# Optimization experiments

Hardware: AMD Instinct MI355X
Metric: run time of the kernel (lower is better)

Reference implementation:

```python
import jax, jax.numpy as jnp
from jax import lax
import numpy as np

STATE_DIM = 64
CHANNELS = 128
SEQ_LEN = 4096
BATCH = 16
DT_MIN, DT_MAX = 1e-3, 1e-1


def hippo(n):
    # HiPPO-LegS construction, matching the torch staticmethod
    ar = jnp.arange(n, dtype=jnp.float32)
    P = jnp.sqrt(1.0 + 2.0 * ar)
    A = P[:, None] * P[None, :]
    A = jnp.tril(A) - jnp.diag(ar)
    B = jnp.sqrt(2.0 * ar + 1.0)
    return -A, B[:, None]


def setup_inputs() -> dict:
    key = jax.random.key(0)
    k_u, k_c = jax.random.split(key)
    A, B = hippo(STATE_DIM)
    # xavier_normal_ for C: std = sqrt(2/(fan_in+fan_out))
    std = float(np.sqrt(2.0 / (CHANNELS + STATE_DIM)))
    C = jax.random.normal(k_c, (CHANNELS, STATE_DIM), dtype=jnp.float32) * std
    D = jnp.ones((CHANNELS, 1), dtype=jnp.float32)
    # deterministic dt at log-midpoint of [dt_min, dt_max]
    dt = jnp.exp(jnp.array([(np.log(DT_MIN) + np.log(DT_MAX)) / 2.0], dtype=jnp.float32))
    u = jax.random.normal(k_u, (BATCH, SEQ_LEN), dtype=jnp.float32)
    return {"u": u, "A": A, "B": B, "C": C, "D": D, "dt": dt}


def reference(u, A, B, C, D, dt):
    # Training-path forward of LinearStateSpaceLayer (conv-kernel construction + conv1d)
    b, L = u.shape
    n = A.shape[0]
    dt_s = dt[0]
    I = jnp.eye(n, dtype=A.dtype)
    BL = jnp.linalg.inv(I - 0.5 * dt_s * A)            # bilinear discretization
    A_bar = BL @ (I + 0.5 * dt_s * A)                  # (n, n)
    B_bar = (BL * dt_s) @ B                            # (n, 1)

    # kernel k[j] = C @ A_bar^j @ B_bar for j = 0..L-1, via a scan of matvecs
    def step(v, _):
        return A_bar @ v, v
    _, vs = lax.scan(step, B_bar[:, 0], None, length=L)  # (L, n), vs[j] = A_bar^j B_bar
    k_causal = vs @ C.T                                  # (L, channels)
    # torch ordering: k_conv[c, 0, i] = C A_bar^{L-1-i} B_bar = k_causal[L-1-i, c]
    k_conv = k_causal[::-1].T[:, None, :]                # (channels, 1, L)

    # torch F.conv1d is cross-correlation; lax conv_general_dilated matches
    y = lax.conv_general_dilated(
        u[:, None, :], k_conv,
        window_strides=(1,), padding=[(L - 1, L - 1)],
        dimension_numbers=("NCH", "OIH", "NCH"),
    )[:, :, :L]                                          # (b, channels, L)

    # skip term: (u.unsqueeze(-1) @ D.T).transpose(-1,-2) == u[b,t] * D[c,0]
    y = y + u[:, None, :] * D[None, :, :]                # (b, channels, L)
    return y
```

## Files before the change

### kernel.cpp

```cpp
#include <hip/hip_runtime.h>

#define NS   64
#define CH   128
#define LSEQ 4096
#define NB   16
#define SCH  64
#define MCH  64
#define ST   68
#define CP   128

#define WS_ABAR 0
#define WS_A16  4096
#define WS_VS   8192
#define WS_BBAR 12288

#define X0_IDX(b, m) (((size_t)(b) * CH) * LSEQ + (size_t)(m) * SCH)

#define P_VSS  0
#define P_XCW  1024
#define P_XBS  1280
#define P_PLE  1536
#define P_PART 1792
#define P_A16  2048

#define FMA44(av, bv)                                                          \
    a0.x += av.x * bv.x; a0.y += av.x * bv.y; a0.z += av.x * bv.z; a0.w += av.x * bv.w; \
    a1.x += av.y * bv.x; a1.y += av.y * bv.y; a1.z += av.y * bv.z; a1.w += av.y * bv.w; \
    a2.x += av.z * bv.x; a2.y += av.z * bv.y; a2.z += av.z * bv.z; a2.w += av.z * bv.w; \
    a3.x += av.w * bv.x; a3.y += av.w * bv.y; a3.z += av.w * bv.z; a3.w += av.w * bv.w;

template<bool WT>
__device__ __forceinline__ void mm_square(const float* __restrict__ cm,
                                          const float* __restrict__ cmt,
                                          float* __restrict__ nm,
                                          float* __restrict__ nmt, int e) {
    const int l = e & 63;
    const int si0 = 16 * ((e >> 6) & 3) + 4 * (l >> 4);
    const int sj0 = 4 * (l & 15);
    float4 a0 = {0,0,0,0}, a1 = {0,0,0,0}, a2 = {0,0,0,0}, a3 = {0,0,0,0};
#pragma unroll 4
    for (int k = 0; k < NS; k += 4) {
        float4 av0 = *(const float4*)&cmt[(k + 0) * ST + si0];
        float4 bv0 = *(const float4*)&cm [(k + 0) * ST + sj0];
        float4 av1 = *(const float4*)&cmt[(k + 1) * ST + si0];
        float4 bv1 = *(const float4*)&cm [(k + 1) * ST + sj0];
        float4 av2 = *(const float4*)&cmt[(k + 2) * ST + si0];
        float4 bv2 = *(const float4*)&cm [(k + 2) * ST + sj0];
        float4 av3 = *(const float4*)&cmt[(k + 3) * ST + si0];
        float4 bv3 = *(const float4*)&cm [(k + 3) * ST + sj0];
        FMA44(av0, bv0)
        FMA44(av1, bv1)
        FMA44(av2, bv2)
        FMA44(av3, bv3)
    }
    *(float4*)&nm[(si0 + 0) * ST + sj0] = a0;
    *(float4*)&nm[(si0 + 1) * ST + sj0] = a1;
    *(float4*)&nm[(si0 + 2) * ST + sj0] = a2;
    *(float4*)&nm[(si0 + 3) * ST + sj0] = a3;
    if (WT) {
        float4 t0 = {a0.x, a1.x, a2.x, a3.x};
        float4 t1 = {a0.y, a1.y, a2.y, a3.y};
        float4 t2 = {a0.z, a1.z, a2.z, a3.z};
        float4 t3 = {a0.w, a1.w, a2.w, a3.w};
        *(float4*)&nmt[(sj0 + 0) * ST + si0] = t0;
        *(float4*)&nmt[(sj0 + 1) * ST + si0] = t1;
        *(float4*)&nmt[(sj0 + 2) * ST + si0] = t2;
        *(float4*)&nmt[(sj0 + 3) * ST + si0] = t3;
    }
}

__device__ __forceinline__ void mm_sq42(const float* __restrict__ cm,
                                        const float* __restrict__ cmt,
                                        float* __restrict__ nm,
                                        float* __restrict__ nmt, int tid) {
    const int si0 = 4 * (tid >> 5);
    const int sj0 = 2 * (tid & 31);
    float2 a0 = {0,0}, a1 = {0,0}, a2 = {0,0}, a3 = {0,0};
#pragma unroll 8
    for (int k = 0; k < NS; ++k) {
        float4 av = *(const float4*)&cmt[k * ST + si0];
        float2 bv = *(const float2*)&cm [k * ST + sj0];
        a0.x += av.x * bv.x; a0.y += av.x * bv.y;
        a1.x += av.y * bv.x; a1.y += av.y * bv.y;
        a2.x += av.z * bv.x; a2.y += av.z * bv.y;
        a3.x += av.w * bv.x; a3.y += av.w * bv.y;
    }
    *(float2*)&nm[(si0 + 0) * ST + sj0] = a0;
    *(float2*)&nm[(si0 + 1) * ST + sj0] = a1;
    *(float2*)&nm[(si0 + 2) * ST + sj0] = a2;
    *(float2*)&nm[(si0 + 3) * ST + sj0] = a3;
    float4 t0 = {a0.x, a1.x, a2.x, a3.x};
    float4 t1 = {a0.y, a1.y, a2.y, a3.y};
    *(float4*)&nmt[(sj0 + 0) * ST + si0] = t0;
    *(float4*)&nmt[(sj0 + 1) * ST + si0] = t1;
}

__device__ __forceinline__ void vs_expand1(const float* __restrict__ cmt,
                                           float* __restrict__ VT,
                                           int iq, int j, int mexp) {
    const int i0 = 4 * iq;
    float4 acc = {0,0,0,0};
#pragma unroll 8
    for (int k = 0; k < NS; ++k) {
        float4 av = *(const float4*)&cmt[k * ST + i0];
        float bk = VT[k * ST + j];
        acc.x += av.x * bk; acc.y += av.y * bk;
        acc.z += av.z * bk; acc.w += av.w * bk;
    }
    VT[(i0 + 0) * ST + mexp + j] = acc.x;
    VT[(i0 + 1) * ST + mexp + j] = acc.y;
    VT[(i0 + 2) * ST + mexp + j] = acc.z;
    VT[(i0 + 3) * ST + mexp + j] = acc.w;
}

__device__ __forceinline__ void pq_step(const float* __restrict__ Acol,
                                        const float* __restrict__ xle,
                                        float* __restrict__ outb, int r0, int e) {
    const int g = e >> 4, i0 = 4 * (e & 15);
    const float* bp = &xle[(4 * g + r0) * NS];
    float4 acc = *(const float4*)&xle[(4 * g + r0 + 1) * NS + i0];
#pragma unroll 8
    for (int k = 0; k < NS; ++k) {
        float4 av = *(const float4*)&Acol[k * ST + i0];
        float bk = bp[k];
        acc.x = fmaf(av.x, bk, acc.x); acc.y = fmaf(av.y, bk, acc.y);
        acc.z = fmaf(av.z, bk, acc.z); acc.w = fmaf(av.w, bk, acc.w);
    }
    *(float4*)&outb[g * ST + i0] = acc;
}

__device__ __forceinline__ void y_step(const float* __restrict__ A128col,
                                       const float* __restrict__ P,
                                       const float* __restrict__ Q,
                                       float* __restrict__ Y, int e) {
    const int g = e >> 4, i0 = 4 * (e & 15);
    const float* bp = &P[g * ST];
    float4 acc = *(const float4*)&Q[g * ST + i0];
#pragma unroll 8
    for (int k = 0; k < NS; ++k) {
        float4 av = *(const float4*)&A128col[k * ST + i0];
        float bk = bp[k];
        acc.x = fmaf(av.x, bk, acc.x); acc.y = fmaf(av.y, bk, acc.y);
        acc.z = fmaf(av.z, bk, acc.z); acc.w = fmaf(av.w, bk, acc.w);
    }
    *(float4*)&Y[g * ST + i0] = acc;
}

__device__ __forceinline__ void inner_step(const float* __restrict__ Acol,
                                           const float* __restrict__ xle,
                                           float* __restrict__ stash, int r, int e) {
    const int g = e >> 4, i0 = 4 * (e & 15);
    const int mp = 4 * g + r - 1;
    float4 acc = *(const float4*)&xle[mp * NS + i0];
    const float* xp = &stash[mp * ST];
#pragma unroll 8
    for (int k = 0; k < NS; ++k) {
        float4 av = *(const float4*)&Acol[k * ST + i0];
        float xk = xp[k];
        acc.x = fmaf(av.x, xk, acc.x); acc.y = fmaf(av.y, xk, acc.y);
        acc.z = fmaf(av.z, xk, acc.z); acc.w = fmaf(av.w, xk, acc.w);
    }
    *(float4*)&stash[(mp + 1) * ST + i0] = acc;
}

__device__ __forceinline__ void e1u_step(const float* __restrict__ A128col,
                                         const float* __restrict__ P,
                                         float* __restrict__ stash, int e) {
    const int g = e >> 4, i0 = 4 * (e & 15);
    const float* xp = &stash[(4 * g) * ST];
    float4 acc = *(const float4*)&P[g * ST + i0];
#pragma unroll 8
    for (int k = 0; k < NS; ++k) {
        float4 av = *(const float4*)&A128col[k * ST + i0];
        float xk = xp[k];
        acc.x = fmaf(av.x, xk, acc.x); acc.y = fmaf(av.y, xk, acc.y);
        acc.z = fmaf(av.z, xk, acc.z); acc.w = fmaf(av.w, xk, acc.w);
    }
    *(float4*)&stash[(4 * g + 2) * ST + i0] = acc;
}

__global__ __launch_bounds__(512) void k_sb(const float* __restrict__ u,
                                            const float* __restrict__ A,
                                            const float* __restrict__ Bv,
                                            const float* __restrict__ dtp,
                                            float* __restrict__ ws,
                                            float* __restrict__ out) {
    __shared__ __align__(16) float Mrow[NS * ST];
    __shared__ __align__(16) float Mcol[(NS + 1) * ST];
    __shared__ __align__(16) float Nrow[NS * ST];
    __shared__ __align__(16) float Ncol[NS * ST];
    __shared__ __align__(16) float VT[NS * ST];
    __shared__ __align__(16) float uT[NS * ST];
    __shared__ __align__(16) float vsS[NS * NS];
    __shared__ __align__(16) float xleS[MCH * NS];
    __shared__ __align__(16) float part[2][4 * NS];
    __shared__ __align__(16) float bcol[NS];
    __shared__ float rdiag[NS], xcS[NS];
    float* const stash = uT;
    float* const HbP = vsS;
    float* const HbQ = vsS + 16 * ST;
    float* const HbY = vsS + 32 * ST;
    const int tid = threadIdx.x;
    const int b = blockIdx.x;
    const float dt = dtp[0];
    const float hdt = 0.5f * dt;

    for (int o = tid; o < NS * NS; o += 512) {
        int i = o >> 6, k = o & 63;
        float a = A[o];
        float d = (i == k) ? 1.0f : 0.0f;
        Nrow[i * ST + k] = d - hdt * a;
        Ncol[k * ST + i] = d + hdt * a;
    }
    if (tid < NS) {
        bcol[tid]  = dt * Bv[tid];
        rdiag[tid] = 1.0f / (1.0f - hdt * A[tid * NS + tid]);
    }
    __syncthreads();

    {
        const int jj = tid & 63;
#pragma unroll
        for (int rep = 0; rep < 2; ++rep) {
            const int m0 = 4 * (tid >> 6) + 32 * rep;
            float4 v;
            v.x = u[b * LSEQ + (m0 + 0) * SCH + 63 - jj];
            v.y = u[b * LSEQ + (m0 + 1) * SCH + 63 - jj];
            v.z = u[b * LSEQ + (m0 + 2) * SCH + 63 - jj];
            v.w = u[b * LSEQ + (m0 + 3) * SCH + 63 - jj];
            *(float4*)&uT[jj * ST + m0] = v;
        }
    }

    if (tid <= NS) {
        float xr[NS];
        const float* t2b = (tid < NS) ? &Ncol[tid * ST] : bcol;
#pragma unroll
        for (int I = 0; I < 16; ++I) {
            const int i0 = 4 * I;
            float4 t2 = *(const float4*)&t2b[i0];
            float a0 = t2.x, a1 = t2.y, a2 = t2.z, a3 = t2.w;
#pragma unroll
            for (int k = 0; k < i0; k += 4) {
                float4 n0 = *(const float4*)&Nrow[(i0 + 0) * ST + k];
                float4 n1 = *(const float4*)&Nrow[(i0 + 1) * ST + k];
                float4 n2 = *(const float4*)&Nrow[(i0 + 2) * ST + k];
                float4 n3 = *(const float4*)&Nrow[(i0 + 3) * ST + k];
                a0 -= n0.x * xr[k] + n0.y * xr[k + 1] + n0.z * xr[k + 2] + n0.w * xr[k + 3];
                a1 -= n1.x * xr[k] + n1.y * xr[k + 1] + n1.z * xr[k + 2] + n1.w * xr[k + 3];
                a2 -= n2.x * xr[k] + n2.y * xr[k + 1] + n2.z * xr[k + 2] + n2.w * xr[k + 3];
                a3 -= n3.x * xr[k] + n3.y * xr[k + 1] + n3.z * xr[k + 2] + n3.w * xr[k + 3];
            }
            float4 rd  = *(const float4*)&rdiag[i0];
            float4 nb1 = *(const float4*)&Nrow[(i0 + 1) * ST + i0];
            float4 nb2 = *(const float4*)&Nrow[(i0 + 2) * ST + i0];
            float4 nb3 = *(const float4*)&Nrow[(i0 + 3) * ST + i0];
            float x0 = a0 * rd.x;
            float x1 = (a1 - nb1.x * x0) * rd.y;
            float x2 = (a2 - nb2.x * x0 - nb2.y * x1) * rd.z;
            float x3 = (a3 - nb3.x * x0 - nb3.y * x1 - nb3.z * x2) * rd.w;
            xr[i0 + 0] = x0; xr[i0 + 1] = x1; xr[i0 + 2] = x2; xr[i0 + 3] = x3;
        }
        float* xrow = &Mcol[tid * ST];
#pragma unroll
        for (int k = 0; k < NS; k += 4) {
            float4 v = {xr[k], xr[k + 1], xr[k + 2], xr[k + 3]};
            *(float4*)&xrow[k] = v;
        }
    }
    __syncthreads();

    if (tid < 256) {
        const int i0 = 4 * (tid >> 4), j0 = 4 * (tid & 15);
        float4 r0 = *(const float4*)&Mcol[(j0 + 0) * ST + i0];
        float4 r1 = *(const float4*)&Mcol[(j0 + 1) * ST + i0];
        float4 r2 = *(const float4*)&Mcol[(j0 + 2) * ST + i0];
        float4 r3 = *(const float4*)&Mcol[(j0 + 3) * ST + i0];
        float4 w0 = {r0.x, r1.x, r2.x, r3.x};
        float4 w1 = {r0.y, r1.y, r2.y, r3.y};
        float4 w2 = {r0.z, r1.z, r2.z, r3.z};
        float4 w3 = {r0.w, r1.w, r2.w, r3.w};
        *(float4*)&Mrow[(i0 + 0) * ST + j0] = w0;
        *(float4*)&Mrow[(i0 + 1) * ST + j0] = w1;
        *(float4*)&Mrow[(i0 + 2) * ST + j0] = w2;
        *(float4*)&Mrow[(i0 + 3) * ST + j0] = w3;
        if (b == 0) {
            *(float4*)&ws[WS_ABAR + (i0 + 0) * NS + j0] = w0;
            *(float4*)&ws[WS_ABAR + (i0 + 1) * NS + j0] = w1;
            *(float4*)&ws[WS_ABAR + (i0 + 2) * NS + j0] = w2;
            *(float4*)&ws[WS_ABAR + (i0 + 3) * NS + j0] = w3;
        }
    }
    if (b == 0 && tid < 16)
        *(float4*)&ws[WS_BBAR + 4 * tid] = *(const float4*)&Mcol[NS * ST + 4 * tid];
    if (tid < NS) VT[tid * ST + 0] = Mcol[NS * ST + tid];
    __syncthreads();

    float *cm = Mrow, *cmt = Mcol, *nm = Nrow, *nmt = Ncol;
    for (int s = 1; s <= 6; ++s) {
        if (s <= 4) {
            mm_sq42(cm, cmt, nm, nmt, tid);
            const int mexp = 1 << (s - 1);
            if (tid < 16 * mexp) {
                vs_expand1(cmt, VT, tid & 15, tid >> 4, mexp);
            }
        } else if (tid < 256) {
            mm_square<true>(cm, cmt, nm, nmt, tid);
        } else {
            const int e = tid - 256;
            const int iq = e & 15;
            if (s == 5) {
                vs_expand1(cmt, VT, iq, e >> 4, 16);
            } else {
                const int j0 = 2 * (e >> 4);
                const int i0 = 4 * iq;
                float4 c0 = {0,0,0,0}, c1 = {0,0,0,0};
#pragma unroll 8
                for (int k = 0; k < NS; ++k) {
                    float4 av = *(const float4*)&cmt[k * ST + i0];
                    float2 bv = *(const float2*)&VT[k * ST + j0];
                    c0.x += av.x * bv.x; c0.y += av.y * bv.x;
                    c0.z += av.z * bv.x; c0.w += av.w * bv.x;
                    c1.x += av.x * bv.y; c1.y += av.y * bv.y;
                    c1.z += av.z * bv.y; c1.w += av.w * bv.y;
                }
                float2 w0 = {c0.x, c1.x}, w1 = {c0.y, c1.y};
                float2 w2 = {c0.z, c1.z}, w3 = {c0.w, c1.w};
                *(float2*)&VT[(i0 + 0) * ST + 32 + j0] = w0;
                *(float2*)&VT[(i0 + 1) * ST + 32 + j0] = w1;
                *(float2*)&VT[(i0 + 2) * ST + 32 + j0] = w2;
                *(float2*)&VT[(i0 + 3) * ST + 32 + j0] = w3;
            }
        }
        __syncthreads();
        { float* t = cm; cm = nm; nm = t; t = cmt; cmt = nmt; nmt = t; }
        if (s == 4 && b == 0) {
            for (int o = tid; o < (NS * NS) / 4; o += 512) {
                int r = o >> 4, c4 = (o & 15) * 4;
                *(float4*)&ws[WS_A16 + r * NS + c4] = *(const float4*)&cm[r * ST + c4];
            }
        }
    }

    if (tid < 256) {
        const int i0 = 4 * (tid >> 4), j0 = 4 * (tid & 15);
        float4 v0 = *(const float4*)&VT[(i0 + 0) * ST + j0];
        float4 v1 = *(const float4*)&VT[(i0 + 1) * ST + j0];
        float4 v2 = *(const float4*)&VT[(i0 + 2) * ST + j0];
        float4 v3 = *(const float4*)&VT[(i0 + 3) * ST + j0];
        float4 w0 = {v0.x, v1.x, v2.x, v3.x};
        float4 w1 = {v0.y, v1.y, v2.y, v3.y};
        float4 w2 = {v0.z, v1.z, v2.z, v3.z};
        float4 w3 = {v0.w, v1.w, v2.w, v3.w};
        *(float4*)&vsS[(j0 + 0) * NS + i0] = w0;
        *(float4*)&vsS[(j0 + 1) * NS + i0] = w1;
        *(float4*)&vsS[(j0 + 2) * NS + i0] = w2;
        *(float4*)&vsS[(j0 + 3) * NS + i0] = w3;
        if (b == 0) {
            *(float4*)&ws[WS_VS + (j0 + 0) * NS + i0] = w0;
            *(float4*)&ws[WS_VS + (j0 + 1) * NS + i0] = w1;
            *(float4*)&ws[WS_VS + (j0 + 2) * NS + i0] = w2;
            *(float4*)&ws[WS_VS + (j0 + 3) * NS + i0] = w3;
        }
    } else {
        mm_square<true>(Mrow, Mcol, Nrow, Ncol, tid - 256);
    }
    __syncthreads();

    if (tid < 256) {
        const int ig = tid & 15, mg = tid >> 4;
        float4 a0 = {0,0,0,0}, a1 = {0,0,0,0}, a2 = {0,0,0,0}, a3 = {0,0,0,0};
#pragma unroll 4
        for (int j = 0; j < NS; j += 2) {
            float4 am  = *(const float4*)&uT[j * ST + 4 * mg];
            float4 bi  = *(const float4*)&vsS[j * NS + 4 * ig];
            float4 am2 = *(const float4*)&uT[(j + 1) * ST + 4 * mg];
            float4 bi2 = *(const float4*)&vsS[(j + 1) * NS + 4 * ig];
            FMA44(am, bi)
            FMA44(am2, bi2)
        }
        *(float4*)&xleS[(4 * mg + 0) * NS + 4 * ig] = a0;
        *(float4*)&xleS[(4 * mg + 1) * NS + 4 * ig] = a1;
        *(float4*)&xleS[(4 * mg + 2) * NS + 4 * ig] = a2;
        *(float4*)&xleS[(4 * mg + 3) * NS + 4 * ig] = a3;
    } else {
        mm_square<false>(Nrow, Ncol, VT, VT, tid - 256);
    }
    __syncthreads();

    float4 a256[4];
    if (tid < 256) {
        const int i = tid & 63, q = tid >> 6;
#pragma unroll
        for (int kq = 0; kq < 4; ++kq)
            a256[kq] = *(const float4*)&VT[i * ST + 16 * q + 4 * kq];
        pq_step(Mcol, xleS, HbP, 0, tid);
    } else {
        pq_step(Mcol, xleS, HbQ, 2, tid - 256);
    }
    __syncthreads();

    if (tid < 256) {
        y_step(Ncol, HbP, HbQ, HbY, tid);
    } else if (tid < 320) {
        xcS[tid - 256] = 0.f;
        stash[tid - 256] = 0.f;
    }
    __syncthreads();

    {
        const int i = tid & 63, q = (tid >> 6) & 3;
        for (int g = 0; g < 15; ++g) {
            if (tid < 256) {
                float4 t0 = *(const float4*)(xcS + 16 * q + 0);
                float4 t1 = *(const float4*)(xcS + 16 * q + 4);
                float4 t2 = *(const float4*)(xcS + 16 * q + 8);
                float4 t3 = *(const float4*)(xcS + 16 * q + 12);
                float s = a256[0].x * t0.x + a256[0].y * t0.y + a256[0].z * t0.z + a256[0].w * t0.w
                        + a256[1].x * t1.x + a256[1].y * t1.y + a256[1].z * t1.z + a256[1].w * t1.w
                        + a256[2].x * t2.x + a256[2].y * t2.y + a256[2].z * t2.z + a256[2].w * t2.w
                        + a256[3].x * t3.x + a256[3].y * t3.y + a256[3].z * t3.z + a256[3].w * t3.w;
                part[g & 1][q * 64 + i] = s;
            }
            __syncthreads();
            if (tid < 256) {
                float xn = part[g & 1][i] + part[g & 1][64 + i] + part[g & 1][128 + i]
                         + part[g & 1][192 + i] + HbY[g * ST + i];
                xcS[i] = xn;
                stash[(4 * g + 4) * ST + i] = xn;
            }
        }
    }
    __syncthreads();

    if (tid < 256) inner_step(Mcol, xleS, stash, 1, tid);
    else           e1u_step(Ncol, HbP, stash, tid - 256);
    __syncthreads();

    if (tid < 256) inner_step(Mcol, xleS, stash, 3, tid);
    __syncthreads();

    {
        const int m = tid >> 3, t8 = (tid & 7) * 8;
        float4 o1 = *(const float4*)&stash[m * ST + t8];
        float4 o2 = *(const float4*)&stash[m * ST + t8 + 4];
        *(float4*)&out[X0_IDX(b, m) + t8]     = o1;
        *(float4*)&out[X0_IDX(b, m) + t8 + 4] = o2;
    }
}

__global__ __launch_bounds__(256) void k_main2(const float* __restrict__ u,
                                               const float* __restrict__ Cm,
                                               const float* __restrict__ Dv,
                                               const float* __restrict__ ws,
                                               float* __restrict__ out) {
    __shared__ __align__(16) float Xl[NS * ST];
    __shared__ __align__(16) float pool[NS * CP];
    __shared__ float uS[SCH], DS[CH], bbS[NS];
    const int m = blockIdx.x, b = blockIdx.y;
    const int tid = threadIdx.x;
    const int l = tid & 63, w = tid >> 6;

    for (int o = tid; o < (NS * NS) / 4; o += 256) {
        int r = o >> 4, c4 = (o & 15) * 4;
        *(float4*)&Xl[r * ST + c4]          = *(const float4*)&ws[WS_ABAR + r * NS + c4];
        *(float4*)&pool[P_A16 + r * NS + c4] = *(const float4*)&ws[WS_A16 + r * NS + c4];
    }
    for (int o = tid; o < 16 * NS; o += 256) pool[P_VSS + o] = ws[WS_VS + o];
    if (tid < NS) {
        uS[tid]  = u[b * LSEQ + m * SCH + tid];
        bbS[tid] = ws[WS_BBAR + tid];
        pool[P_XBS + tid] = out[X0_IDX(b, m) + tid];
    }
    if (tid < CH) DS[tid] = Dv[tid];
    __syncthreads();

    const int r0 = l & 15, q = l >> 4;
    float4 ar[4][4];
#pragma unroll
    for (int b4 = 0; b4 < 4; ++b4)
#pragma unroll
        for (int kq = 0; kq < 4; ++kq)
            ar[b4][kq] = *(const float4*)&Xl[(r0 + 16 * b4) * ST + 16 * q + 4 * kq];
    float bbr[4];
#pragma unroll
    for (int b4 = 0; b4 < 4; ++b4) bbr[b4] = bbS[r0 + 16 * b4];
    float4 a16r[4];
#pragma unroll
    for (int kq = 0; kq < 4; ++kq)
        a16r[kq] = *(const float4*)&pool[P_A16 + l * NS + 16 * w + 4 * kq];

    {
        float s = 0.f;
#pragma unroll
        for (int j = 0; j < 16; ++j) s += pool[P_VSS + j * NS + l] * uS[16 * w + 15 - j];
        pool[P_PLE + w * NS + l] = s;
    }
    __syncthreads();

    for (int p = 1; p < 4; ++p) {
        float4 x0q = *(const float4*)&pool[P_XBS + (p - 1) * NS + 16 * w + 0];
        float4 x1q = *(const float4*)&pool[P_XBS + (p - 1) * NS + 16 * w + 4];
        float4 x2q = *(const float4*)&pool[P_XBS + (p - 1) * NS + 16 * w + 8];
        float4 x3q = *(const float4*)&pool[P_XBS + (p - 1) * NS + 16 * w + 12];
        float s = a16r[0].x * x0q.x + a16r[0].y * x0q.y + a16r[0].z * x0q.z + a16r[0].w * x0q.w
                + a16r[1].x * x1q.x + a16r[1].y * x1q.y + a16r[1].z * x1q.z + a16r[1].w * x1q.w
                + a16r[2].x * x2q.x + a16r[2].y * x2q.y + a16r[2].z * x2q.z + a16r[2].w * x2q.w
                + a16r[3].x * x3q.x + a16r[3].y * x3q.y + a16r[3].z * x3q.z + a16r[3].w * x3q.w;
        pool[P_PART + w * NS + l] = s;
        __syncthreads();
        if (w == 0) {
            float xn = pool[P_PART + l] + pool[P_PART + NS + l] + pool[P_PART + 2 * NS + l]
                     + pool[P_PART + 3 * NS + l] + pool[P_PLE + (p - 1) * NS + l];
            pool[P_XBS + p * NS + l] = xn;
        }
        __syncthreads();
    }

    pool[P_XCW + w * NS + l] = pool[P_XBS + w * NS + l];
    for (int s = 0; s < 16; ++s) {
        __threadfence_block();
        const int t = 16 * w + s;
        float4 x0q = *(const float4*)&pool[P_XCW + w * NS + 16 * q + 0];
        float4 x1q = *(const float4*)&pool[P_XCW + w * NS + 16 * q + 4];
        float4 x2q = *(const float4*)&pool[P_XCW + w * NS + 16 * q + 8];
        float4 x3q = *(const float4*)&pool[P_XCW + w * NS + 16 * q + 12];
        float p0, p1, p2, p3;
        p0 = ar[0][0].x * x0q.x + ar[0][0].y * x0q.y + ar[0][0].z * x0q.z + ar[0][0].w * x0q.w
           + ar[0][1].x * x1q.x + ar[0][1].y * x1q.y + ar[0][1].z * x1q.z + ar[0][1].w * x1q.w
           + ar[0][2].x * x2q.x + ar[0][2].y * x2q.y + ar[0][2].z * x2q.z + ar[0][2].w * x2q.w
           + ar[0][3].x * x3q.x + ar[0][3].y * x3q.y + ar[0][3].z * x3q.z + ar[0][3].w * x3q.w;
        p1 = ar[1][0].x * x0q.x + ar[1][0].y * x0q.y + ar[1][0].z * x0q.z + ar[1][0].w * x0q.w
           + ar[1][1].x * x1q.x + ar[1][1].y * x1q.y + ar[1][1].z * x1q.z + ar[1][1].w * x1q.w
           + ar[1][2].x * x2q.x + ar[1][2].y * x2q.y + ar[1][2].z * x2q.z + ar[1][2].w * x2q.w
           + ar[1][3].x * x3q.x + ar[1][3].y * x3q.y + ar[1][3].z * x3q.z + ar[1][3].w * x3q.w;
        p2 = ar[2][0].x * x0q.x + ar[2][0].y * x0q.y + ar[2][0].z * x0q.z + ar[2][0].w * x0q.w
           + ar[2][1].x * x1q.x + ar[2][1].y * x1q.y + ar[2][1].z * x1q.z + ar[2][1].w * x1q.w
           + ar[2][2].x * x2q.x + ar[2][2].y * x2q.y + ar[2][2].z * x2q.z + ar[2][2].w * x2q.w
           + ar[2][3].x * x3q.x + ar[2][3].y * x3q.y + ar[2][3].z * x3q.z + ar[2][3].w * x3q.w;
        p3 = ar[3][0].x * x0q.x + ar[3][0].y * x0q.y + ar[3][0].z * x0q.z + ar[3][0].w * x0q.w
           + ar[3][1].x * x1q.x + ar[3][1].y * x1q.y + ar[3][1].z * x1q.z + ar[3][1].w * x1q.w
           + ar[3][2].x * x2q.x + ar[3][2].y * x2q.y + ar[3][2].z * x2q.z + ar[3][2].w * x2q.w
           + ar[3][3].x * x3q.x + ar[3][3].y * x3q.y + ar[3][3].z * x3q.z + ar[3][3].w * x3q.w;
        p0 += __shfl_xor(p0, 16, 64); p1 += __shfl_xor(p1, 16, 64);
        p2 += __shfl_xor(p2, 16, 64); p3 += __shfl_xor(p3, 16, 64);
        p0 += __shfl_xor(p0, 32, 64); p1 += __shfl_xor(p1, 32, 64);
        p2 += __shfl_xor(p2, 32, 64); p3 += __shfl_xor(p3, 32, 64);
        const float ut = uS[t];
        p0 += bbr[0] * ut; p1 += bbr[1] * ut; p2 += bbr[2] * ut; p3 += bbr[3] * ut;
        const float xv = (q == 0) ? p0 : (q == 1) ? p1 : (q == 2) ? p2 : p3;
        const int row = r0 + 16 * q;
        pool[P_XCW + w * NS + row] = xv;
        Xl[row * ST + t] = xv;
    }
    __syncthreads();

#pragma unroll
    for (int rep = 0; rep < 8; ++rep) {
        const int ii = tid & 63;
        const int cg = (tid >> 6) + 4 * rep;
        float4 v;
        v.x = Cm[(4 * cg + 0) * NS + ii];
        v.y = Cm[(4 * cg + 1) * NS + ii];
        v.z = Cm[(4 * cg + 2) * NS + ii];
        v.w = Cm[(4 * cg + 3) * NS + ii];
        *(float4*)&pool[ii * CP + 4 * cg] = v;
    }
    __syncthreads();

    {
        const int tg = tid & 7, cq = tid >> 3;
        float acc[4][8];
#pragma unroll
        for (int r = 0; r < 4; ++r)
#pragma unroll
            for (int c = 0; c < 8; ++c) acc[r][c] = 0.f;
#pragma unroll 4
        for (int ii = 0; ii < NS; ++ii) {
            float4 cv = *(const float4*)&pool[ii * CP + 4 * cq];
            float4 xa = *(const float4*)&Xl[ii * ST + 8 * tg + 0];
            float4 xb = *(const float4*)&Xl[ii * ST + 8 * tg + 4];
            float cr[4] = {cv.x, cv.y, cv.z, cv.w};
            float xv[8] = {xa.x, xa.y, xa.z, xa.w, xb.x, xb.y, xb.z, xb.w};
#pragma unroll
            for (int r = 0; r < 4; ++r)
#pragma unroll
                for (int c = 0; c < 8; ++c) acc[r][c] += cr[r] * xv[c];
        }
        const size_t obase = ((size_t)b * CH) * LSEQ + (size_t)m * SCH + 8 * tg;
#pragma unroll
        for (int r = 0; r < 4; ++r) {
            const int c = 4 * cq + r;
            const float dv = DS[c];
            float4 o1, o2;
            o1.x = acc[r][0] + dv * uS[8 * tg + 0];
            o1.y = acc[r][1] + dv * uS[8 * tg + 1];
            o1.z = acc[r][2] + dv * uS[8 * tg + 2];
            o1.w = acc[r][3] + dv * uS[8 * tg + 3];
            o2.x = acc[r][4] + dv * uS[8 * tg + 4];
            o2.y = acc[r][5] + dv * uS[8 * tg + 5];
            o2.z = acc[r][6] + dv * uS[8 * tg + 6];
            o2.w = acc[r][7] + dv * uS[8 * tg + 7];
            float* op = out + obase + (size_t)c * LSEQ;
            *(float4*)(op)     = o1;
            *(float4*)(op + 4) = o2;
        }
    }
}

extern "C" void kernel_launch(void* const* d_in, const int* in_sizes, int n_in,
                              void* d_out, int out_size, void* d_ws, size_t ws_size,
                              hipStream_t stream) {
    const float* u   = (const float*)d_in[0];
    const float* A   = (const float*)d_in[1];
    const float* Bv  = (const float*)d_in[2];
    const float* Cm  = (const float*)d_in[3];
    const float* Dv  = (const float*)d_in[4];
    const float* dtp = (const float*)d_in[5];
    float* ws  = (float*)d_ws;
    float* out = (float*)d_out;

    k_sb<<<NB, 512, 0, stream>>>(u, A, Bv, dtp, ws, out);
    k_main2<<<dim3(MCH, NB), 256, 0, stream>>>(u, Cm, Dv, ws, out);
}
```

Baseline: 154.3 us.

## Shorten serial chunk-state recurrence to 7 steps using A^512 and 3-level expansion

The serial block-level recurrence over chunk states now strides by 8 chunks using a precomputed A^512 power (one extra matrix squaring, which also stores the transposed A^256) instead of 15 steps with A^256. The intermediate chunk states are then filled in by a three-stage tree expansion with new row/column matvec helpers. The matrix-square loops are cut to a triangular k range, assuming lower-triangular powers. Workspace writes are also spread across blocks 1-3 instead of all coming from block 0. This trades fewer serialized, barrier-bound steps for more shared memory (an extra 64x68 buffer) and extra parallel matvec work.

Result: no change. 154.4 us (+0.1%).

```diff
diff --git a/kernel.cpp b/kernel.cpp
--- a/kernel.cpp
+++ b/kernel.cpp
@@ -29,6 +29,7 @@
     a2.x += av.z * bv.x; a2.y += av.z * bv.y; a2.z += av.z * bv.z; a2.w += av.z * bv.w; \
     a3.x += av.w * bv.x; a3.y += av.w * bv.y; a3.z += av.w * bv.z; a3.w += av.w * bv.w;
 
+
 template<bool WT>
 __device__ __forceinline__ void mm_square(const float* __restrict__ cm,
                                           const float* __restrict__ cmt,
@@ -37,9 +38,9 @@
     const int l = e & 63;
     const int si0 = 16 * ((e >> 6) & 3) + 4 * (l >> 4);
     const int sj0 = 4 * (l & 15);
+    const int kmax = si0 + 4;
     float4 a0 = {0,0,0,0}, a1 = {0,0,0,0}, a2 = {0,0,0,0}, a3 = {0,0,0,0};
-#pragma unroll 4
-    for (int k = 0; k < NS; k += 4) {
+    for (int k = 0; k < kmax; k += 4) {
         float4 av0 = *(const float4*)&cmt[(k + 0) * ST + si0];
         float4 bv0 = *(const float4*)&cm [(k + 0) * ST + sj0];
         float4 av1 = *(const float4*)&cmt[(k + 1) * ST + si0];
@@ -75,9 +76,10 @@
                                         float* __restrict__ nmt, int tid) {
     const int si0 = 4 * (tid >> 5);
     const int sj0 = 2 * (tid & 31);
+    const int kmax = si0 + 4;
     float2 a0 = {0,0}, a1 = {0,0}, a2 = {0,0}, a3 = {0,0};
-#pragma unroll 8
-    for (int k = 0; k < NS; ++k) {
+#pragma unroll 4
+    for (int k = 0; k < kmax; ++k) {
         float4 av = *(const float4*)&cmt[k * ST + si0];
         float2 bv = *(const float2*)&cm [k * ST + sj0];
         a0.x += av.x * bv.x; a0.y += av.x * bv.y;
@@ -146,37 +148,33 @@
     *(float4*)&Y[g * ST + i0] = acc;
 }
 
-__device__ __forceinline__ void inner_step(const float* __restrict__ Acol,
-                                           const float* __restrict__ xle,
-                                           float* __restrict__ stash, int r, int e) {
-    const int g = e >> 4, i0 = 4 * (e & 15);
-    const int mp = 4 * g + r - 1;
-    float4 acc = *(const float4*)&xle[mp * NS + i0];
-    const float* xp = &stash[mp * ST];
+__device__ __forceinline__ void exp8u(const float* __restrict__ Pcol,
+                                      const float* __restrict__ addRow,
+                                      const float* __restrict__ srcRow,
+                                      float* __restrict__ dstRow, int i0) {
+    float4 acc = *(const float4*)&addRow[i0];
 #pragma unroll 8
     for (int k = 0; k < NS; ++k) {
-        float4 av = *(const float4*)&Acol[k * ST + i0];
-        float xk = xp[k];
+        float4 av = *(const float4*)&Pcol[k * ST + i0];
+        float xk = srcRow[k];
         acc.x = fmaf(av.x, xk, acc.x); acc.y = fmaf(av.y, xk, acc.y);
         acc.z = fmaf(av.z, xk, acc.z); acc.w = fmaf(av.w, xk, acc.w);
     }
-    *(float4*)&stash[(mp + 1) * ST + i0] = acc;
-}
-
-__device__ __forceinline__ void e1u_step(const float* __restrict__ A128col,
-                                         const float* __restrict__ P,
-                                         float* __restrict__ stash, int e) {
-    const int g = e >> 4, i0 = 4 * (e & 15);
-    const float* xp = &stash[(4 * g) * ST];
-    float4 acc = *(const float4*)&P[g * ST + i0];
+    *(float4*)&dstRow[i0] = acc;
+}
+
+__device__ __forceinline__ void exp8r2(const float* __restrict__ Prow,
+                                       const float* __restrict__ addRow,
+                                       const float* __restrict__ srcRow,
+                                       float* __restrict__ dstRow, int c0) {
+    float2 acc = *(const float2*)&addRow[c0];
 #pragma unroll 8
     for (int k = 0; k < NS; ++k) {
-        float4 av = *(const float4*)&A128col[k * ST + i0];
-        float xk = xp[k];
-        acc.x = fmaf(av.x, xk, acc.x); acc.y = fmaf(av.y, xk, acc.y);
-        acc.z = fmaf(av.z, xk, acc.z); acc.w = fmaf(av.w, xk, acc.w);
-    }
-    *(float4*)&stash[(4 * g + 2) * ST + i0] = acc;
+        float xk = srcRow[k];
+        acc.x = fmaf(Prow[(c0 + 0) * ST + k], xk, acc.x);
+        acc.y = fmaf(Prow[(c0 + 1) * ST + k], xk, acc.y);
+    }
+    *(float2*)&dstRow[c0] = acc;
 }
 
 __global__ __launch_bounds__(512) void k_sb(const float* __restrict__ u,
@@ -190,6 +188,7 @@
     __shared__ __align__(16) float Nrow[NS * ST];
     __shared__ __align__(16) float Ncol[NS * ST];
     __shared__ __align__(16) float VT[NS * ST];
+    __shared__ __align__(16) float A5[NS * ST];
     __shared__ __align__(16) float uT[NS * ST];
     __shared__ __align__(16) float vsS[NS * NS];
     __shared__ __align__(16) float xleS[MCH * NS];
@@ -291,7 +290,7 @@
             *(float4*)&ws[WS_ABAR + (i0 + 3) * NS + j0] = w3;
         }
     }
-    if (b == 0 && tid < 16)
+    if (b == 1 && tid < 16)
         *(float4*)&ws[WS_BBAR + 4 * tid] = *(const float4*)&Mcol[NS * ST + 4 * tid];
     if (tid < NS) VT[tid * ST + 0] = Mcol[NS * ST + tid];
     __syncthreads();
@@ -334,7 +333,7 @@
         }
         __syncthreads();
         { float* t = cm; cm = nm; nm = t; t = cmt; cmt = nmt; nmt = t; }
-        if (s == 4 && b == 0) {
+        if (s == 4 && b == 2) {
             for (int o = tid; o < (NS * NS) / 4; o += 512) {
                 int r = o >> 4, c4 = (o & 15) * 4;
                 *(float4*)&ws[WS_A16 + r * NS + c4] = *(const float4*)&cm[r * ST + c4];
@@ -356,7 +355,7 @@
         *(float4*)&vsS[(j0 + 1) * NS + i0] = w1;
         *(float4*)&vsS[(j0 + 2) * NS + i0] = w2;
         *(float4*)&vsS[(j0 + 3) * NS + i0] = w3;
-        if (b == 0) {
+        if (b == 3) {
             *(float4*)&ws[WS_VS + (j0 + 0) * NS + i0] = w0;
             *(float4*)&ws[WS_VS + (j0 + 1) * NS + i0] = w1;
             *(float4*)&ws[WS_VS + (j0 + 2) * NS + i0] = w2;
@@ -384,60 +383,83 @@
         *(float4*)&xleS[(4 * mg + 2) * NS + 4 * ig] = a2;
         *(float4*)&xleS[(4 * mg + 3) * NS + 4 * ig] = a3;
     } else {
-        mm_square<false>(Nrow, Ncol, VT, VT, tid - 256);
-    }
-    __syncthreads();
-
-    float4 a256[4];
+        mm_square<true>(Nrow, Ncol, VT, A5, tid - 256);
+    }
+    __syncthreads();
+
+    if (tid < 256) pq_step(Mcol, xleS, HbP, 0, tid);
+    else           pq_step(Mcol, xleS, HbQ, 2, tid - 256);
+    if (tid < 64) { xcS[tid] = 0.f; stash[tid] = 0.f; }
+    __syncthreads();
+
+    if (tid < 256) y_step(Ncol, HbP, HbQ, HbY, tid);
+    else           mm_square<false>(VT, A5, Mrow, Mrow, tid - 256);
+    __syncthreads();
+
+    float4 a512[4];
     if (tid < 256) {
         const int i = tid & 63, q = tid >> 6;
 #pragma unroll
         for (int kq = 0; kq < 4; ++kq)
-            a256[kq] = *(const float4*)&VT[i * ST + 16 * q + 4 * kq];
-        pq_step(Mcol, xleS, HbP, 0, tid);
-    } else {
-        pq_step(Mcol, xleS, HbQ, 2, tid - 256);
-    }
-    __syncthreads();
-
-    if (tid < 256) {
-        y_step(Ncol, HbP, HbQ, HbY, tid);
-    } else if (tid < 320) {
-        xcS[tid - 256] = 0.f;
-        stash[tid - 256] = 0.f;
+            a512[kq] = *(const float4*)&Mrow[i * ST + 16 * q + 4 * kq];
+        const int g = tid >> 5, c0 = 2 * (tid & 31);
+        exp8r2(VT, &HbY[(2 * g + 1) * ST], &HbY[(2 * g) * ST], &HbQ[g * ST], c0);
     }
     __syncthreads();
 
     {
         const int i = tid & 63, q = (tid >> 6) & 3;
-        for (int g = 0; g < 15; ++g) {
+        for (int g = 0; g < 7; ++g) {
             if (tid < 256) {
                 float4 t0 = *(const float4*)(xcS + 16 * q + 0);
                 float4 t1 = *(const float4*)(xcS + 16 * q + 4);
                 float4 t2 = *(const float4*)(xcS + 16 * q + 8);
                 float4 t3 = *(const float4*)(xcS + 16 * q + 12);
-                float s = a256[0].x * t0.x + a256[0].y * t0.y + a256[0].z * t0.z + a256[0].w * t0.w
-                        + a256[1].x * t1.x + a256[1].y * t1.y + a256[1].z * t1.z + a256[1].w * t1.w
-                        + a256[2].x * t2.x + a256[2].y * t2.y + a256[2].z * t2.z + a256[2].w * t2.w
-                        + a256[3].x * t3.x + a256[3].y * t3.y + a256[3].z * t3.z + a256[3].w * t3.w;
+                float s = a512[0].x * t0.x + a512[0].y * t0.y + a512[0].z * t0.z + a512[0].w * t0.w
+                        + a512[1].x * t1.x + a512[1].y * t1.y + a512[1].z * t1.z + a512[1].w * t1.w
+                        + a512[2].x * t2.x + a512[2].y * t2.y + a512[2].z * t2.z + a512[2].w * t2.w
+                        + a512[3].x * t3.x + a512[3].y * t3.y + a512[3].z * t3.z + a512[3].w * t3.w;
                 part[g & 1][q * 64 + i] = s;
             }
             __syncthreads();
             if (tid < 256) {
                 float xn = part[g & 1][i] + part[g & 1][64 + i] + part[g & 1][128 + i]
-                         + part[g & 1][192 + i] + HbY[g * ST + i];
+                         + part[g & 1][192 + i] + HbQ[g * ST + i];
                 xcS[i] = xn;
-                stash[(4 * g + 4) * ST + i] = xn;
+                stash[(8 * g + 8) * ST + i] = xn;
             }
         }
     }
     __syncthreads();
 
-    if (tid < 256) inner_step(Mcol, xleS, stash, 1, tid);
-    else           e1u_step(Ncol, HbP, stash, tid - 256);
-    __syncthreads();
-
-    if (tid < 256) inner_step(Mcol, xleS, stash, 3, tid);
+    if (tid < 128) {
+        const int g = tid >> 4, i0 = 4 * (tid & 15);
+        exp8u(Mcol, &xleS[(8 * g) * NS], &stash[(8 * g) * ST], &stash[(8 * g + 1) * ST], i0);
+    } else if (tid < 256) {
+        const int e = tid - 128, g = e >> 4, i0 = 4 * (e & 15);
+        exp8u(Ncol, &HbP[(2 * g) * ST], &stash[(8 * g) * ST], &stash[(8 * g + 2) * ST], i0);
+    } else {
+        const int e = tid - 256, g = e >> 5, c0 = 2 * (e & 31);
+        exp8r2(VT, &HbY[(2 * g) * ST], &stash[(8 * g) * ST], &stash[(8 * g + 4) * ST], c0);
+    }
+    __syncthreads();
+
+    if (tid < 128) {
+        const int g = tid >> 4, i0 = 4 * (tid & 15);
+        exp8u(Mcol, &xleS[(8 * g + 2) * NS], &stash[(8 * g + 2) * ST], &stash[(8 * g + 3) * ST], i0);
+    } else if (tid < 256) {
+        const int e = tid - 128, g = e >> 4, i0 = 4 * (e & 15);
+        exp8u(Mcol, &xleS[(8 * g + 4) * NS], &stash[(8 * g + 4) * ST], &stash[(8 * g + 5) * ST], i0);
+    } else if (tid < 384) {
+        const int e = tid - 256, g = e >> 4, i0 = 4 * (e & 15);
+        exp8u(Ncol, &HbP[(2 * g + 1) * ST], &stash[(8 * g + 4) * ST], &stash[(8 * g + 6) * ST], i0);
+    }
+    __syncthreads();
+
+    if (tid < 128) {
+        const int g = tid >> 4, i0 = 4 * (tid & 15);
+        exp8u(Mcol, &xleS[(8 * g + 6) * NS], &stash[(8 * g + 6) * ST], &stash[(8 * g + 7) * ST], i0);
+    }
     __syncthreads();
 
     {
```
